# Kernel optimization log

Hardware: AMD Instinct MI355X
Metric: run time of the kernel (lower is better)

Reference implementation:

```python
import jax, jax.numpy as jnp
import numpy as np


def setup_inputs() -> dict:
    key = jax.random.key(0)
    k0, k1, k2 = jax.random.split(key, 3)
    G, E, C, H, F = 8, 8, 512, 1024, 4096
    inputs = jax.random.normal(k0, (G, E, C, H), dtype=jnp.float32)
    # TruncatedNormal(stddev=0.02) initializer approximated by scaled normal
    wi = jax.random.normal(k1, (E, H, F), dtype=jnp.float32) * 0.02
    bi = jnp.zeros((E, F), dtype=jnp.float32)
    wo = jax.random.normal(k2, (E, F, H), dtype=jnp.float32) * 0.02
    bo = jnp.zeros((E, H), dtype=jnp.float32)
    return {"inputs": inputs, "wi": wi, "bi": bi, "wo": wo, "bo": bo}


def reference(inputs, wi, bi, wo, bo):
    # intermediate: gech,ehf->gecf + bias[e,f]
    x = jnp.einsum('gech,ehf->gecf', inputs, wi) + bi[None, :, None, :]
    x = jax.nn.gelu(x, approximate=False)  # keras gelu default is exact
    # output: gecf,efh->gech + bias[e,h]
    x = jnp.einsum('gecf,efh->gech', x, wo) + bo[None, :, None, :]
    # dropout is identity at inference (training=None)
    return x
```

## Files before the change

kernel.cpp:

```cpp
#include <hip/hip_runtime.h>
#include <hip/hip_bf16.h>
#include <math.h>

#define GG 8
#define EE 8
#define CC 512
#define HH 1024
#define FF 4096

typedef __attribute__((ext_vector_type(8))) short bf16x8;
typedef __attribute__((ext_vector_type(4))) float f32x4;

__device__ __forceinline__ unsigned short f2bf(float f) {
  unsigned int u = __float_as_uint(f);
  u += 0x7FFFu + ((u >> 16) & 1u);
  return (unsigned short)(u >> 16);
}

__device__ __forceinline__ void gload_lds16(const void* g, void* l) {
  __builtin_amdgcn_global_load_lds((__attribute__((address_space(1))) void*)g,
                                   (__attribute__((address_space(3))) void*)l,
                                   16, 0, 0);
}

__device__ __forceinline__ float fast_gelu(float x) {
  const float u = x * (1.5957691216057308f + 0.0713548162726009f * x * x);
  return x / (1.0f + __expf(-u));
}

__global__ void convert_bf16_kernel(const float4* __restrict__ in,
                                    ushort4* __restrict__ out) {
  const int i = blockIdx.x * blockDim.x + threadIdx.x;
  const float4 v = in[i];
  ushort4 o;
  o.x = f2bf(v.x); o.y = f2bf(v.y); o.z = f2bf(v.z); o.w = f2bf(v.w);
  out[i] = o;
}

__global__ void transpose_bf16(const float* __restrict__ in,
                               unsigned short* __restrict__ out,
                               int R, int C) {
  __shared__ float tile[64][65];
  const long ebase = (long)blockIdx.z * R * C;
  const int r0 = blockIdx.y * 64, c0 = blockIdx.x * 64;
  const int t = threadIdx.x;
  const int lr = t >> 4;
  const int lc = (t & 15) * 4;
#pragma unroll
  for (int p = 0; p < 4; ++p) {
    const int r = lr + p * 16;
    const float4 v = *(const float4*)(in + ebase + (long)(r0 + r) * C + c0 + lc);
    tile[r][lc + 0] = v.x; tile[r][lc + 1] = v.y;
    tile[r][lc + 2] = v.z; tile[r][lc + 3] = v.w;
  }
  __syncthreads();
#pragma unroll
  for (int p = 0; p < 4; ++p) {
    const int c = lr + p * 16;
    ushort4 o;
    o.x = f2bf(tile[lc + 0][c]);
    o.y = f2bf(tile[lc + 1][c]);
    o.z = f2bf(tile[lc + 2][c]);
    o.w = f2bf(tile[lc + 3][c]);
    *(ushort4*)(out + ebase + (long)(c0 + c) * R + r0 + lc) = o;
  }
}

template <int GELU>
__global__ __launch_bounds__(256, 2)
void ffn_gemm(const unsigned short* __restrict__ A,
              const unsigned short* __restrict__ Bt,
              const float* __restrict__ bias,
              void* __restrict__ Out,
              int K, int N) {
  __shared__ __align__(16) union SMem {
    struct { unsigned short As[128 * 32]; unsigned short Bs[128 * 32]; } s;
    unsigned short ep[4 * 32 * 68];
  } smem;
  unsigned short* As = smem.s.As;
  unsigned short* Bs = smem.s.Bs;

  const int z = blockIdx.z;
  const int g = z & 7;
  const int e = z >> 3;
  const long mBase = (long)(g * EE + e) * 512 + blockIdx.y * 128;
  const int nBase = blockIdx.x * 128;

  const unsigned short* Ab = A + mBase * K;
  const unsigned short* Bb = Bt + ((long)e * N + nBase) * K;

  const int tid = threadIdx.x;
  const int lane = tid & 63;
  const int wave = tid >> 6;
  const int wm = wave & 1, wn = wave >> 1;
  const int q = lane >> 4, mn = lane & 15;
  const int srow = lane >> 2, sb = lane & 3;

  f32x4 acc[4][4] = {};

  for (int k0 = 0; k0 < K; k0 += 32) {
    __syncthreads();
#pragma unroll
    for (int j = 0; j < 2; ++j) {
      const int ca = wave + j * 4;
      const int row = ca * 16 + srow;
      const int kb = (sb ^ ((row >> 1) & 3)) * 8;
      gload_lds16(Ab + (long)row * K + k0 + kb, &As[ca * 512 + lane * 8]);
      gload_lds16(Bb + (long)row * K + k0 + kb, &Bs[ca * 512 + lane * 8]);
    }
    __syncthreads();

    bf16x8 af[4], bfr[4];
#pragma unroll
    for (int t = 0; t < 4; ++t) {
      const int m = wm * 64 + t * 16 + mn;
      af[t] = *(const bf16x8*)&As[m * 32 + ((q ^ ((m >> 1) & 3)) * 8)];
      const int n = wn * 64 + t * 16 + mn;
      bfr[t] = *(const bf16x8*)&Bs[n * 32 + ((q ^ ((n >> 1) & 3)) * 8)];
    }
#pragma unroll
    for (int mt = 0; mt < 4; ++mt)
#pragma unroll
      for (int nt = 0; nt < 4; ++nt)
        acc[mt][nt] = __builtin_amdgcn_mfma_f32_16x16x32_bf16(
            af[mt], bfr[nt], acc[mt][nt], 0, 0, 0);
  }

  if (GELU) {
    __syncthreads();
    unsigned short* ep = &smem.ep[wave * (32 * 68)];
    unsigned short* outp = (unsigned short*)Out;
#pragma unroll
    for (int p2 = 0; p2 < 2; ++p2) {
#pragma unroll
      for (int mt = 2 * p2; mt < 2 * p2 + 2; ++mt) {
#pragma unroll
        for (int nt = 0; nt < 4; ++nt) {
          const int n = nBase + wn * 64 + nt * 16 + mn;
          const float bv = bias[(long)e * N + n];
#pragma unroll
          for (int r = 0; r < 4; ++r) {
            const int lr = (mt - 2 * p2) * 16 + q * 4 + r;
            const float v = fast_gelu(acc[mt][nt][r] + bv);
            ep[lr * 68 + nt * 16 + mn] = f2bf(v);
          }
        }
      }
      const int c4 = (lane & 15) * 4;
#pragma unroll
      for (int i = 0; i < 8; ++i) {
        const int lr2 = i * 4 + (lane >> 4);
        const ushort4 v = *(const ushort4*)&ep[lr2 * 68 + c4];
        const long m = mBase + wm * 64 + p2 * 32 + lr2;
        *(ushort4*)&outp[m * N + nBase + wn * 64 + c4] = v;
      }
    }
  } else {
#pragma unroll
    for (int nt = 0; nt < 4; ++nt) {
      const int n = nBase + wn * 64 + nt * 16 + mn;
      const float bv = bias[(long)e * N + n];
#pragma unroll
      for (int mt = 0; mt < 4; ++mt) {
#pragma unroll
        for (int r = 0; r < 4; ++r) {
          const long m = mBase + wm * 64 + mt * 16 + q * 4 + r;
          ((float*)Out)[m * N + n] = acc[mt][nt][r] + bv;
        }
      }
    }
  }
}

extern "C" void kernel_launch(void* const* d_in, const int* in_sizes, int n_in,
                              void* d_out, int out_size, void* d_ws, size_t ws_size,
                              hipStream_t stream) {
  const float* x  = (const float*)d_in[0];
  const float* wi = (const float*)d_in[1];
  const float* bi = (const float*)d_in[2];
  const float* wo = (const float*)d_in[3];
  const float* bo = (const float*)d_in[4];
  float* out = (float*)d_out;

  char* ws = (char*)d_ws;
  unsigned short* xb = (unsigned short*)ws;
  unsigned short* yb = (unsigned short*)(ws + (size_t)64 * 1024 * 1024);
  unsigned short* wt = (unsigned short*)(ws + (size_t)320 * 1024 * 1024);

  convert_bf16_kernel<<<32768, 256, 0, stream>>>((const float4*)x, (ushort4*)xb);

  transpose_bf16<<<dim3(FF / 64, HH / 64, EE), 256, 0, stream>>>(wi, wt, HH, FF);

  ffn_gemm<1><<<dim3(FF / 128, 4, GG * EE), 256, 0, stream>>>(xb, wt, bi, yb, HH, FF);

  transpose_bf16<<<dim3(HH / 64, FF / 64, EE), 256, 0, stream>>>(wo, wt, FF, HH);

  ffn_gemm<0><<<dim3(HH / 128, 4, GG * EE), 256, 0, stream>>>(yb, wt, bo, out, FF, HH);
}
```

Measured before the change: 1.137 ms.

## Double-buffer GEMM with 256x256 tiles, 512 threads and interleaved prefetch

Rewrites the FFN GEMM kernel to use 256x256 output tiles with 8 waves. LDS staging is now double-buffered over 64-wide K steps, and the async global->LDS loads for the next tile are interleaved with MFMA phases using explicit barriers, waitcnt and setprio. It also switches to an XOR-swizzled LDS layout and makes K/N template constants. The goal is to hide memory latency and raise arithmetic intensity per block, at the cost of more registers and LDS, which may reduce occupancy.

```diff
diff --git a/kernel.cpp b/kernel.cpp
--- a/kernel.cpp
+++ b/kernel.cpp
@@ -66,106 +66,178 @@
   }
 }
 
-template <int GELU>
-__global__ __launch_bounds__(256, 2)
+
+#define SWZ(o) ((o) ^ ((((o) >> 7) & 7) << 4))
+
+#define BARp() __builtin_amdgcn_s_barrier()
+#define LGKM0() do { asm volatile("s_waitcnt lgkmcnt(0)" ::: "memory"); \
+                     __builtin_amdgcn_sched_barrier(0); } while (0)
+#define VMC(n) asm volatile("s_waitcnt vmcnt(" #n ")" ::: "memory")
+
+#define STAGE_A(bf, kh, kt) do { \
+    const long _kb = ((long)(kt) * 64 + (kh) * 32) * 2; \
+    char* _d = (char*)&sm.s.A[bf][kh][0]; \
+    gload_lds16(Ab + (long)sr0 * K2 + _kb + sc0, _d + p0); \
+    gload_lds16(Ab + (long)sr1 * K2 + _kb + sc1, _d + p1); \
+  } while (0)
+
+#define STAGE_B(bf, kh, kt) do { \
+    const long _kb = ((long)(kt) * 64 + (kh) * 32) * 2; \
+    char* _d = (char*)&sm.s.B[bf][kh][0]; \
+    gload_lds16(Bb + (long)sr0 * K2 + _kb + sc0, _d + p0); \
+    gload_lds16(Bb + (long)sr1 * K2 + _kb + sc1, _d + p1); \
+  } while (0)
+
+#define LDA_(bf, kh) do { \
+    const char* _p = (const char*)&sm.s.A[bf][kh][0]; \
+    _Pragma("unroll") \
+    for (int _m = 0; _m < 8; ++_m) { \
+      const int _r = wm * 128 + _m * 16 + mn; \
+      const int _o = SWZ((_r << 6) | (q << 4)); \
+      a_fr[_m] = *(const bf16x8*)(_p + _o); \
+    } \
+  } while (0)
+
+#define LDB_(bf, kh, np) do { \
+    const char* _p = (const char*)&sm.s.B[bf][kh][0]; \
+    _Pragma("unroll") \
+    for (int _j = 0; _j < 2; ++_j) { \
+      const int _r = wn * 64 + ((np) * 2 + _j) * 16 + mn; \
+      const int _o = SWZ((_r << 6) | (q << 4)); \
+      b_fr[_j] = *(const bf16x8*)(_p + _o); \
+    } \
+  } while (0)
+
+#define MFMA_(np) do { \
+    __builtin_amdgcn_s_setprio(1); \
+    _Pragma("unroll") \
+    for (int _m = 0; _m < 8; ++_m) { \
+      acc[_m][(np) * 2 + 0] = __builtin_amdgcn_mfma_f32_16x16x32_bf16( \
+          a_fr[_m], b_fr[0], acc[_m][(np) * 2 + 0], 0, 0, 0); \
+      acc[_m][(np) * 2 + 1] = __builtin_amdgcn_mfma_f32_16x16x32_bf16( \
+          a_fr[_m], b_fr[1], acc[_m][(np) * 2 + 1], 0, 0, 0); \
+    } \
+    __builtin_amdgcn_s_setprio(0); \
+  } while (0)
+
+template <int GELU, int K, int N>
+__global__ __launch_bounds__(512, 2)
 void ffn_gemm(const unsigned short* __restrict__ A,
               const unsigned short* __restrict__ Bt,
               const float* __restrict__ bias,
-              void* __restrict__ Out,
-              int K, int N) {
+              void* __restrict__ Out) {
   __shared__ __align__(16) union SMem {
-    struct { unsigned short As[128 * 32]; unsigned short Bs[128 * 32]; } s;
-    unsigned short ep[4 * 32 * 68];
-  } smem;
-  unsigned short* As = smem.s.As;
-  unsigned short* Bs = smem.s.Bs;
+    struct {
+      unsigned short A[2][2][256 * 32];
+      unsigned short B[2][2][256 * 32];
+    } s;
+    unsigned short ep[8][32 * 68];
+  } sm;
 
   const int z = blockIdx.z;
   const int g = z & 7;
   const int e = z >> 3;
-  const long mBase = (long)(g * EE + e) * 512 + blockIdx.y * 128;
-  const int nBase = blockIdx.x * 128;
-
-  const unsigned short* Ab = A + mBase * K;
-  const unsigned short* Bb = Bt + ((long)e * N + nBase) * K;
+  const long mBase = (long)(g * EE + e) * 512 + blockIdx.y * 256;
+  const int nBase = blockIdx.x * 256;
+
+  const char* Ab = (const char*)(A + mBase * (long)K);
+  const char* Bb = (const char*)(Bt + ((long)e * N + nBase) * (long)K);
+  const long K2 = (long)K * 2;
 
   const int tid = threadIdx.x;
-  const int lane = tid & 63;
-  const int wave = tid >> 6;
-  const int wm = wave & 1, wn = wave >> 1;
-  const int q = lane >> 4, mn = lane & 15;
-  const int srow = lane >> 2, sb = lane & 3;
-
-  f32x4 acc[4][4] = {};
-
-  for (int k0 = 0; k0 < K; k0 += 32) {
-    __syncthreads();
-#pragma unroll
-    for (int j = 0; j < 2; ++j) {
-      const int ca = wave + j * 4;
-      const int row = ca * 16 + srow;
-      const int kb = (sb ^ ((row >> 1) & 3)) * 8;
-      gload_lds16(Ab + (long)row * K + k0 + kb, &As[ca * 512 + lane * 8]);
-      gload_lds16(Bb + (long)row * K + k0 + kb, &Bs[ca * 512 + lane * 8]);
-    }
-    __syncthreads();
-
-    bf16x8 af[4], bfr[4];
-#pragma unroll
-    for (int t = 0; t < 4; ++t) {
-      const int m = wm * 64 + t * 16 + mn;
-      af[t] = *(const bf16x8*)&As[m * 32 + ((q ^ ((m >> 1) & 3)) * 8)];
-      const int n = wn * 64 + t * 16 + mn;
-      bfr[t] = *(const bf16x8*)&Bs[n * 32 + ((q ^ ((n >> 1) & 3)) * 8)];
-    }
-#pragma unroll
-    for (int mt = 0; mt < 4; ++mt)
-#pragma unroll
-      for (int nt = 0; nt < 4; ++nt)
-        acc[mt][nt] = __builtin_amdgcn_mfma_f32_16x16x32_bf16(
-            af[mt], bfr[nt], acc[mt][nt], 0, 0, 0);
-  }
+  const int lane = tid & 63, wave = tid >> 6;
+  const int wm = wave >> 2, wn = wave & 3;
+  const int mn = lane & 15, q = lane >> 4;
+
+  const int p0 = tid * 16, p1 = p0 + 8192;
+  const int o0 = SWZ(p0), o1 = SWZ(p1);
+  const int sr0 = o0 >> 6, sc0 = o0 & 63;
+  const int sr1 = o1 >> 6, sc1 = o1 & 63;
+
+  bf16x8 a_fr[8];
+  bf16x8 b_fr[2];
+  f32x4 acc[8][4] = {};
+
+  STAGE_A(0, 0, 0); STAGE_B(0, 0, 0); STAGE_A(0, 1, 0); STAGE_B(0, 1, 0);
+  VMC(4);
+  BARp();
+
+  constexpr int KT = K / 64;
+#pragma unroll 2
+  for (int t = 0; t < KT; ++t) {
+    const int cur = t & 1, nxt = cur ^ 1;
+    const int ktn = (t + 1 == KT) ? 0 : t + 1;
+
+    LDA_(cur, 0);
+    LDB_(cur, 0, 0);
+    STAGE_A(nxt, 0, ktn);
+    BARp(); LGKM0();
+    MFMA_(0);
+    BARp();
+    LDB_(cur, 0, 1);
+    STAGE_B(nxt, 0, ktn);
+    VMC(4);
+    BARp(); LGKM0();
+    MFMA_(1);
+    BARp();
+    LDA_(cur, 1);
+    LDB_(cur, 1, 0);
+    STAGE_A(nxt, 1, ktn);
+    BARp(); LGKM0();
+    MFMA_(0);
+    BARp();
+    LDB_(cur, 1, 1);
+    STAGE_B(nxt, 1, ktn);
+    VMC(4);
+    BARp(); LGKM0();
+    MFMA_(1);
+    BARp();
+  }
+
+  asm volatile("s_waitcnt vmcnt(0)" ::: "memory");
+  __syncthreads();
 
   if (GELU) {
-    __syncthreads();
-    unsigned short* ep = &smem.ep[wave * (32 * 68)];
+    unsigned short* ep = &sm.ep[wave][0];
     unsigned short* outp = (unsigned short*)Out;
 #pragma unroll
-    for (int p2 = 0; p2 < 2; ++p2) {
-#pragma unroll
-      for (int mt = 2 * p2; mt < 2 * p2 + 2; ++mt) {
+    for (int p2 = 0; p2 < 4; ++p2) {
+#pragma unroll
+      for (int mtL = 0; mtL < 2; ++mtL) {
+        const int mt = 2 * p2 + mtL;
 #pragma unroll
         for (int nt = 0; nt < 4; ++nt) {
           const int n = nBase + wn * 64 + nt * 16 + mn;
           const float bv = bias[(long)e * N + n];
 #pragma unroll
           for (int r = 0; r < 4; ++r) {
-            const int lr = (mt - 2 * p2) * 16 + q * 4 + r;
+            const int lr = mtL * 16 + q * 4 + r;
             const float v = fast_gelu(acc[mt][nt][r] + bv);
             ep[lr * 68 + nt * 16 + mn] = f2bf(v);
           }
         }
       }
-      const int c4 = (lane & 15) * 4;
+      const int c4 = mn * 4;
 #pragma unroll
       for (int i = 0; i < 8; ++i) {
-        const int lr2 = i * 4 + (lane >> 4);
+        const int lr2 = i * 4 + q;
         const ushort4 v = *(const ushort4*)&ep[lr2 * 68 + c4];
-        const long m = mBase + wm * 64 + p2 * 32 + lr2;
+        const long m = mBase + wm * 128 + p2 * 32 + lr2;
         *(ushort4*)&outp[m * N + nBase + wn * 64 + c4] = v;
       }
     }
   } else {
+    float* outp = (float*)Out;
 #pragma unroll
     for (int nt = 0; nt < 4; ++nt) {
       const int n = nBase + wn * 64 + nt * 16 + mn;
       const float bv = bias[(long)e * N + n];
 #pragma unroll
-      for (int mt = 0; mt < 4; ++mt) {
+      for (int mt = 0; mt < 8; ++mt) {
 #pragma unroll
         for (int r = 0; r < 4; ++r) {
-          const long m = mBase + wm * 64 + mt * 16 + q * 4 + r;
-          ((float*)Out)[m * N + n] = acc[mt][nt][r] + bv;
+          const long m = mBase + wm * 128 + mt * 16 + q * 4 + r;
+          outp[m * N + n] = acc[mt][nt][r] + bv;
         }
       }
     }
@@ -191,9 +263,9 @@
 
   transpose_bf16<<<dim3(FF / 64, HH / 64, EE), 256, 0, stream>>>(wi, wt, HH, FF);
 
-  ffn_gemm<1><<<dim3(FF / 128, 4, GG * EE), 256, 0, stream>>>(xb, wt, bi, yb, HH, FF);
+  ffn_gemm<1, HH, FF><<<dim3(FF / 256, CC / 256, GG * EE), 512, 0, stream>>>(xb, wt, bi, yb);
 
   transpose_bf16<<<dim3(HH / 64, FF / 64, EE), 256, 0, stream>>>(wo, wt, FF, HH);
 
-  ffn_gemm<0><<<dim3(HH / 128, 4, GG * EE), 256, 0, stream>>>(yb, wt, bo, out, FF, HH);
-}
+  ffn_gemm<0, FF, HH><<<dim3(HH / 256, CC / 256, GG * EE), 512, 0, stream>>>(yb, wt, bo, out);
+}
```

Measured after the change: 1.002 ms. 1.13x faster.
